# Optimization experiments

Measured on AMD Instinct MI355X. Metric: run time of the kernel, lower is better.

Reference implementation:

```python
import jax, jax.numpy as jnp
import numpy as np

VOCAB = 32000; D_MODEL = 768; N_LAYERS = 4
D_STATE = 16; D_CONV = 4; EXPAND = 2
D_INNER = EXPAND * D_MODEL                 # 1536
DT_RANK = (D_MODEL + 15) // 16             # 48
BATCH = 2; SEQ = 1024


def setup_inputs():
    key = jax.random.key(0)
    ks = jax.random.split(key, 10)
    def nrm(k, shape, scale=0.02):
        return (jax.random.normal(k, shape) * scale).astype(jnp.float32)
    inp = {}
    inp['tokens'] = jax.random.randint(ks[0], (BATCH, SEQ), 0, VOCAB)
    inp['embedding'] = nrm(ks[1], (VOCAB, D_MODEL))
    inp['head_bias'] = jnp.zeros((VOCAB,), jnp.float32)
    inp['ln_g'] = jnp.ones((N_LAYERS, D_MODEL), jnp.float32)
    inp['ln_b'] = jnp.zeros((N_LAYERS, D_MODEL), jnp.float32)
    inp['W_in'] = nrm(ks[2], (N_LAYERS, 2 * D_INNER, D_MODEL))
    inp['conv_w'] = nrm(ks[3], (N_LAYERS, D_INNER, 1, D_CONV), 0.1)
    inp['conv_b'] = jnp.zeros((N_LAYERS, D_INNER), jnp.float32)
    inp['W_xproj'] = nrm(ks[4], (N_LAYERS, DT_RANK + 2 * D_STATE, D_INNER))
    inp['W_dt'] = nrm(ks[5], (N_LAYERS, D_INNER, DT_RANK), 0.1)
    inp['b_dt'] = nrm(ks[6], (N_LAYERS, D_INNER), 0.5)
    # S4D-real init: A_n = n for n in 1..d_state
    inp['A_log'] = jnp.broadcast_to(jnp.log(jnp.arange(1, D_STATE + 1, dtype=jnp.float32)), (N_LAYERS, D_INNER, D_STATE)).copy()
    inp['D_ssm'] = jnp.ones((N_LAYERS, D_INNER), jnp.float32)
    inp['W_out'] = nrm(ks[7], (N_LAYERS, D_MODEL, D_INNER))
    inp['norm_g'] = jnp.ones((D_MODEL,), jnp.float32)
    inp['norm_b'] = jnp.zeros((D_MODEL,), jnp.float32)
    return inp


def _ln(x, g, b):
    m = jnp.mean(x, axis=-1, keepdims=True)
    v = jnp.var(x, axis=-1, keepdims=True)
    return (x - m) * jax.lax.rsqrt(v + 1e-5) * g + b


def _mamba(x, W_in, conv_w, conv_b, W_xproj, W_dt, b_dt, A_log, D_ssm, W_out):
    # x: (S, B, D_MODEL)
    xz = jnp.einsum('sbd,ed->sbe', x, W_in)           # (S, B, 2*D_INNER)
    xc, z = jnp.split(xz, 2, axis=-1)
    # depthwise causal conv along sequence
    xt = jnp.transpose(xc, (1, 2, 0))                  # (B, C, S)
    xt = jax.lax.conv_general_dilated(xt, conv_w, (1,), [(D_CONV - 1, 0)],
                                      dimension_numbers=('NCH', 'OIH', 'NCH'),
                                      feature_group_count=D_INNER)
    xt = xt + conv_b[None, :, None]
    xc = jax.nn.silu(jnp.transpose(xt, (2, 0, 1)))     # (S, B, C)
    xdb = jnp.einsum('sbc,ec->sbe', xc, W_xproj)       # (S, B, DT_RANK+2N)
    dt_r = xdb[..., :DT_RANK]
    Bm = xdb[..., DT_RANK:DT_RANK + D_STATE]
    Cm = xdb[..., DT_RANK + D_STATE:]
    dt = jax.nn.softplus(jnp.einsum('sbr,cr->sbc', dt_r, W_dt) + b_dt)
    A = -jnp.exp(A_log)                                # (C, N)

    def step(h, t):
        dt_t, B_t, C_t, x_t = t                        # (B,C),(B,N),(B,N),(B,C)
        dA = jnp.exp(dt_t[..., None] * A)              # (B, C, N)
        h = h * dA + (dt_t * x_t)[..., None] * B_t[:, None, :]
        y = jnp.einsum('bcn,bn->bc', h, C_t)
        return h, y

    h0 = jnp.zeros((x.shape[1], D_INNER, D_STATE), x.dtype)
    _, ys = jax.lax.scan(step, h0, (dt, Bm, Cm, xc))   # ys: (S, B, C)
    y = (ys + D_ssm * xc) * jax.nn.silu(z)
    return jnp.einsum('sbc,dc->sbd', y, W_out)


def reference(tokens, embedding, head_bias, ln_g, ln_b, W_in, conv_w, conv_b, W_xproj, W_dt, b_dt, A_log, D_ssm, W_out, norm_g, norm_b):
    x = embedding[tokens.T]                            # (S, B, D)
    for i in range(N_LAYERS):
        x = x + _mamba(_ln(x, ln_g[i], ln_b[i]), W_in[i], conv_w[i], conv_b[i],
                       W_xproj[i], W_dt[i], b_dt[i], A_log[i], D_ssm[i], W_out[i])
    x = _ln(x, norm_g, norm_b)
    logits = jnp.einsum('sbd,vd->sbv', x, embedding) + head_bias  # tied head
    return jnp.transpose(logits, (1, 0, 2))            # (B, S, VOCAB)
```

## Files before the change

kernel.cpp:

```cpp
#include <hip/hip_runtime.h>
#include <hip/hip_bf16.h>
#include <cstdint>
#include <cstddef>

#define SEQ_LEN 1024
#define NBATCH  2
#define MROWS   2048
#define DMODEL  768
#define DINNER  1536
#define DTRANK  48
#define DSTATE  16
#define NLAYERS 4
#define NVOCAB  32000
#define XPROJ_N 80
#define NCHUNK  16
#define CHUNK   64
#define GROUPS  (NBATCH * DINNER)
#define SCANW   (GROUPS * DSTATE)

typedef __attribute__((ext_vector_type(4))) float f32x4;
typedef __attribute__((ext_vector_type(8))) short s16x8;
using bf16 = __hip_bfloat16;

__device__ __forceinline__ float b2f(bf16 v){ return __bfloat162float(v); }
__device__ __forceinline__ bf16  f2b(float v){ return __float2bfloat16(v); }
__device__ __forceinline__ short f2bs(float v){
  return (short)__builtin_bit_cast(unsigned short, __float2bfloat16(v));
}

__device__ __forceinline__ void glds16(const ushort* g, ushort* l) {
  __builtin_amdgcn_global_load_lds(
      (const __attribute__((address_space(1))) void*)g,
      (__attribute__((address_space(3))) void*)l,
      16, 0, 0);
}

__global__ __launch_bounds__(256) void k_cvt(const float* __restrict__ in,
    ushort* __restrict__ out, int n4) {
  int i = blockIdx.x * 256 + threadIdx.x;
  if (i >= n4) return;
  f32x4 v = *(const f32x4*)(in + (size_t)i * 4);
  ushort4 o;
  o.x = (ushort)f2bs(v[0]); o.y = (ushort)f2bs(v[1]);
  o.z = (ushort)f2bs(v[2]); o.w = (ushort)f2bs(v[3]);
  *(ushort4*)(out + (size_t)i * 4) = o;
}

__global__ __launch_bounds__(256) void k_zero(float* __restrict__ p, int n4) {
  int i = blockIdx.x * 256 + threadIdx.x;
  if (i >= n4) return;
  f32x4 z = {};
  *(f32x4*)(p + (size_t)i * 4) = z;
}

__global__ __launch_bounds__(256) void k_embed(const int* __restrict__ tok,
    const float* __restrict__ emb, float* __restrict__ x) {
  int id = blockIdx.x * 256 + threadIdx.x;
  int m = id / DMODEL, d = id - m * DMODEL;
  x[id] = emb[(size_t)tok[m] * DMODEL + d];
}

__global__ __launch_bounds__(256) void k_ln(const float* __restrict__ x,
    bf16* __restrict__ out, const float* __restrict__ g, const float* __restrict__ b) {
  int m = blockIdx.x;
  const float* row = x + (size_t)m * DMODEL;
  int t = threadIdx.x;
  float v0[3];
  float s = 0.f, s2 = 0.f;
#pragma unroll
  for (int j = 0; j < 3; j++) {
    float v = row[t + j * 256];
    v0[j] = v; s += v; s2 += v * v;
  }
#pragma unroll
  for (int o = 32; o >= 1; o >>= 1) { s += __shfl_xor(s, o); s2 += __shfl_xor(s2, o); }
  __shared__ float red[8];
  int wave = t >> 6;
  if ((t & 63) == 0) { red[wave] = s; red[4 + wave] = s2; }
  __syncthreads();
  s  = red[0] + red[1] + red[2] + red[3];
  s2 = red[4] + red[5] + red[6] + red[7];
  float mean = s * (1.f / DMODEL);
  float var  = s2 * (1.f / DMODEL) - mean * mean;
  float rstd = rsqrtf(var + 1e-5f);
#pragma unroll
  for (int j = 0; j < 3; j++) {
    int d = t + j * 256;
    float o = (v0[j] - mean) * rstd * g[d] + b[d];
    out[(size_t)m * DMODEL + d] = f2b(o);
  }
}

template<bool HAS_BIAS, bool ADD_TO_C, bool ATOMIC>
__global__ __launch_bounds__(256) void k_gemm128(
    const ushort* __restrict__ A, int lda,
    const ushort* __restrict__ B, int ldb,
    float* __restrict__ C, int ldc,
    const float* __restrict__ bias,
    int M, int N, int K)
{
  __shared__ ushort As[128 * 32];
  __shared__ ushort Bs[128 * 32];
  const int t = threadIdx.x;
  const int lane = t & 63;
  const int wave = t >> 6;
  const int tile_m = blockIdx.x * 128;
  const int tile_n = blockIdx.y * 128;
  const int kper = K / gridDim.z;
  const int kb = blockIdx.z * kper;
  const int ke = kb + kper;
  const int wr = (wave >> 1) * 64;
  const int wc = (wave & 1) * 64;

  f32x4 acc[4][4] = {};

  const int sr = wave * 32 + (lane >> 2);
  const int sc = (lane & 3) * 8;
  const ushort* gA0 = A + (size_t)(tile_m + sr) * lda + sc + kb;
  const ushort* gA1 = gA0 + (size_t)16 * lda;
  const ushort* gB0 = B + (size_t)(tile_n + sr) * ldb + sc + kb;
  const ushort* gB1 = gB0 + (size_t)16 * ldb;
  ushort* lA0 = As + wave * 1024;
  ushort* lA1 = As + wave * 1024 + 512;
  ushort* lB0 = Bs + wave * 1024;
  ushort* lB1 = Bs + wave * 1024 + 512;

  const int fr = lane & 15;
  const int kk = (lane >> 4) * 8;

  for (int k0 = kb; k0 < ke; k0 += 32) {
    glds16(gA0, lA0);
    glds16(gA1, lA1);
    glds16(gB0, lB0);
    glds16(gB1, lB1);
    gA0 += 32; gA1 += 32; gB0 += 32; gB1 += 32;
    __syncthreads();
    s16x8 a[4], b[4];
#pragma unroll
    for (int m = 0; m < 4; m++)
      a[m] = *(const s16x8*)&As[(wr + m * 16 + fr) * 32 + kk];
#pragma unroll
    for (int n = 0; n < 4; n++)
      b[n] = *(const s16x8*)&Bs[(wc + n * 16 + fr) * 32 + kk];
#pragma unroll
    for (int m = 0; m < 4; m++)
#pragma unroll
      for (int n = 0; n < 4; n++)
        acc[m][n] = __builtin_amdgcn_mfma_f32_16x16x32_bf16(a[m], b[n], acc[m][n], 0, 0, 0);
    __syncthreads();
  }

  const int rq = (lane >> 4) * 4;
#pragma unroll
  for (int m = 0; m < 4; m++)
#pragma unroll
    for (int n = 0; n < 4; n++) {
      int colg = tile_n + wc + n * 16 + fr;
      float bv = HAS_BIAS ? bias[colg] : 0.f;
#pragma unroll
      for (int r = 0; r < 4; r++) {
        int rowg = tile_m + wr + m * 16 + rq + r;
        size_t idx = (size_t)rowg * ldc + colg;
        float v = acc[m][n][r] + bv;
        if constexpr (ATOMIC) atomicAdd(&C[idx], v);
        else if constexpr (ADD_TO_C) C[idx] += v;
        else C[idx] = v;
      }
    }
}

template<int MODE>
__global__ __launch_bounds__(256) void k_gemm(
    const ushort* __restrict__ A, int lda,
    const ushort* __restrict__ W, int ldw,
    void* __restrict__ Cout, int ldc,
    int M, int N, int K,
    const float* __restrict__ bias,
    const float* __restrict__ xcp,
    float* __restrict__ dtxp)
{
  __shared__ ushort As[64][40];
  __shared__ ushort Ws[64][40];
  const int tile_m = blockIdx.x * 64;
  const int tile_n = blockIdx.y * 64;
  const int t = threadIdx.x;
  const int lane = t & 63;
  const int wave = t >> 6;
  const int wr = (wave >> 1) * 32;
  const int wc = (wave & 1) * 32;
  f32x4 acc[2][2] = {};

  const int kper = ((K + gridDim.z - 1) / gridDim.z + 31) & ~31;
  const int kb = blockIdx.z * kper;
  int ke = kb + kper; if (ke > K) ke = K;

  const int srow = t >> 2;
  const int scol = (t & 3) * 8;

  for (int k0 = kb; k0 < ke; k0 += 32) {
    {
      int gm = tile_m + srow, gk = k0 + scol;
      s16x8 v = {};
      if (gm < M) {
        if (gk + 8 <= K) v = *(const s16x8*)(A + (size_t)gm * lda + gk);
        else {
#pragma unroll
          for (int j = 0; j < 8; j++) if (gk + j < K) v[j] = (short)A[(size_t)gm * lda + gk + j];
        }
      }
      *(s16x8*)&As[srow][scol] = v;
    }
    {
      int gn = tile_n + srow, gk = k0 + scol;
      s16x8 v = {};
      if (gn < N) {
        if (gk + 8 <= K) v = *(const s16x8*)(W + (size_t)gn * ldw + gk);
        else {
#pragma unroll
          for (int j = 0; j < 8; j++) if (gk + j < K) v[j] = (short)W[(size_t)gn * ldw + gk + j];
        }
      }
      *(s16x8*)&Ws[srow][scol] = v;
    }
    __syncthreads();
    const int kk = (lane >> 4) * 8;
    const int fr = lane & 15;
    s16x8 a0 = *(const s16x8*)&As[wr + fr][kk];
    s16x8 a1 = *(const s16x8*)&As[wr + 16 + fr][kk];
    s16x8 b0 = *(const s16x8*)&Ws[wc + fr][kk];
    s16x8 b1 = *(const s16x8*)&Ws[wc + 16 + fr][kk];
    acc[0][0] = __builtin_amdgcn_mfma_f32_16x16x32_bf16(a0, b0, acc[0][0], 0, 0, 0);
    acc[0][1] = __builtin_amdgcn_mfma_f32_16x16x32_bf16(a0, b1, acc[0][1], 0, 0, 0);
    acc[1][0] = __builtin_amdgcn_mfma_f32_16x16x32_bf16(a1, b0, acc[1][0], 0, 0, 0);
    acc[1][1] = __builtin_amdgcn_mfma_f32_16x16x32_bf16(a1, b1, acc[1][1], 0, 0, 0);
    __syncthreads();
  }

  const int fr = lane & 15;
  const int rq = (lane >> 4) * 4;
#pragma unroll
  for (int i = 0; i < 2; i++)
#pragma unroll
    for (int j = 0; j < 2; j++) {
      int colg = tile_n + wc + j * 16 + fr;
#pragma unroll
      for (int r = 0; r < 4; r++) {
        int rowg = tile_m + wr + i * 16 + rq + r;
        if (rowg < M && colg < N) {
          float v = acc[i][j][r];
          size_t idx = (size_t)rowg * ldc + colg;
          if constexpr (MODE == 0) {
            ((bf16*)Cout)[idx] = f2b(v);
          } else if constexpr (MODE == 2) {
            v += bias[colg];
            float sp = (v > 20.f) ? v : log1pf(__expf(v));
            ((float*)Cout)[idx] = sp;
            dtxp[idx] = sp * xcp[idx];
          } else {
            atomicAdd((float*)Cout + idx, v);
          }
        }
      }
    }
}

__global__ __launch_bounds__(256) void k_conv(const float* __restrict__ xz,
    const float* __restrict__ w, const float* __restrict__ cb,
    float* __restrict__ xc, bf16* __restrict__ xcb) {
  int id = blockIdx.x * 256 + threadIdx.x;
  int m = id / DINNER, c = id - m * DINNER;
  int s = m & (SEQ_LEN - 1);
  float acc = cb[c];
#pragma unroll
  for (int k = 0; k < 4; k++) {
    int sp = s - 3 + k;
    if (sp >= 0) acc += w[c * 4 + k] * xz[(size_t)(m - 3 + k) * (2 * DINNER) + c];
  }
  float sil = acc / (1.f + __expf(-acc));
  xc[id] = sil;
  xcb[id] = f2b(sil);
}

__global__ __launch_bounds__(256) void k_scan1(const float* __restrict__ dt,
    const float* __restrict__ dtx, const bf16* __restrict__ xdb,
    const float* __restrict__ A_log, float* __restrict__ aprod,
    float* __restrict__ hend) {
  int gid = blockIdx.x * 256 + threadIdx.x;
  int n  = gid & 15;
  int t2 = gid >> 4;
  int j  = t2 / GROUPS;
  int cb = t2 - j * GROUPS;
  int c  = cb % DINNER;
  int b  = cb / DINNER;
  float Acn = -__expf(A_log[c * DSTATE + n]);
  float h = 0.f, ap = 1.f;
  int mbase = b * SEQ_LEN + j * CHUNK;
#pragma unroll 4
  for (int s = 0; s < CHUNK; s++) {
    int m = mbase + s;
    float dtv = dt[(size_t)m * DINNER + c];
    float dxv = dtx[(size_t)m * DINNER + c];
    float Bv  = b2f(xdb[(size_t)m * XPROJ_N + DTRANK + n]);
    float dA  = __expf(dtv * Acn);
    h = h * dA + dxv * Bv;
    ap *= dA;
  }
  aprod[gid] = ap;
  hend[gid]  = h;
}

__global__ __launch_bounds__(256) void k_scan2(const float* __restrict__ aprod,
    const float* __restrict__ hend, float* __restrict__ hin) {
  int idx = blockIdx.x * 256 + threadIdx.x;
  float h = 0.f;
#pragma unroll
  for (int j = 0; j < NCHUNK; j++) {
    hin[(size_t)j * SCANW + idx] = h;
    h = aprod[(size_t)j * SCANW + idx] * h + hend[(size_t)j * SCANW + idx];
  }
}

__global__ __launch_bounds__(256) void k_scan3(const float* __restrict__ dt,
    const float* __restrict__ dtx, const bf16* __restrict__ xdb,
    const float* __restrict__ A_log, const float* __restrict__ hin,
    float* __restrict__ y) {
  int gid = blockIdx.x * 256 + threadIdx.x;
  int n  = gid & 15;
  int t2 = gid >> 4;
  int j  = t2 / GROUPS;
  int cb = t2 - j * GROUPS;
  int c  = cb % DINNER;
  int b  = cb / DINNER;
  float Acn = -__expf(A_log[c * DSTATE + n]);
  float h = hin[gid];
  int mbase = b * SEQ_LEN + j * CHUNK;
#pragma unroll 2
  for (int s = 0; s < CHUNK; s++) {
    int m = mbase + s;
    float dtv = dt[(size_t)m * DINNER + c];
    float dxv = dtx[(size_t)m * DINNER + c];
    float Bv  = b2f(xdb[(size_t)m * XPROJ_N + DTRANK + n]);
    float Cv  = b2f(xdb[(size_t)m * XPROJ_N + DTRANK + DSTATE + n]);
    float dA  = __expf(dtv * Acn);
    h = h * dA + dxv * Bv;
    float p = h * Cv;
    p += __shfl_xor(p, 8);
    p += __shfl_xor(p, 4);
    p += __shfl_xor(p, 2);
    p += __shfl_xor(p, 1);
    if (n == 0) y[(size_t)m * DINNER + c] = p;
  }
}

__global__ __launch_bounds__(256) void k_ycomb(const float* __restrict__ y,
    const float* __restrict__ xc, const float* __restrict__ xz,
    const float* __restrict__ D_ssm, bf16* __restrict__ ybf) {
  int id = blockIdx.x * 256 + threadIdx.x;
  int m = id / DINNER, c = id - m * DINNER;
  float z = xz[(size_t)m * (2 * DINNER) + DINNER + c];
  float sil = z / (1.f + __expf(-z));
  float v = (y[id] + D_ssm[c] * xc[id]) * sil;
  ybf[id] = f2b(v);
}

extern "C" void kernel_launch(void* const* d_in, const int* in_sizes, int n_in,
                              void* d_out, int out_size, void* d_ws, size_t ws_size,
                              hipStream_t stream) {
  const int*   tokens    = (const int*)  d_in[0];
  const float* embedding = (const float*)d_in[1];
  const float* head_bias = (const float*)d_in[2];
  const float* ln_g      = (const float*)d_in[3];
  const float* ln_b      = (const float*)d_in[4];
  const float* W_in      = (const float*)d_in[5];
  const float* conv_w    = (const float*)d_in[6];
  const float* conv_b    = (const float*)d_in[7];
  const float* W_xproj   = (const float*)d_in[8];
  const float* W_dt      = (const float*)d_in[9];
  const float* b_dt      = (const float*)d_in[10];
  const float* A_log     = (const float*)d_in[11];
  const float* D_ssm     = (const float*)d_in[12];
  const float* W_out     = (const float*)d_in[13];
  const float* norm_g    = (const float*)d_in[14];
  const float* norm_b    = (const float*)d_in[15];
  float* out = (float*)d_out;

  char* ws = (char*)d_ws;
  size_t off = 0;
  auto alloc = [&](size_t bytes) -> char* {
    char* p = ws + off;
    off = (off + bytes + 255) & ~(size_t)255;
    return p;
  };
  float*  x     = (float*) alloc((size_t)MROWS * DMODEL * 4);
  bf16*   xln   = (bf16*)  alloc((size_t)MROWS * DMODEL * 2);
  float*  xz    = (float*) alloc((size_t)MROWS * 2 * DINNER * 4);
  float*  xc    = (float*) alloc((size_t)MROWS * DINNER * 4);
  bf16*   xcb   = (bf16*)  alloc((size_t)MROWS * DINNER * 2);
  bf16*   xdb   = (bf16*)  alloc((size_t)MROWS * XPROJ_N * 2);
  float*  xdbf  = (float*) alloc((size_t)MROWS * XPROJ_N * 4);
  float*  dtf   = (float*) alloc((size_t)MROWS * DINNER * 4);
  float*  dtx   = (float*) alloc((size_t)MROWS * DINNER * 4);
  float*  yraw  = (float*) alloc((size_t)MROWS * DINNER * 4);
  bf16*   ybf   = (bf16*)  alloc((size_t)MROWS * DINNER * 2);
  float*  aprod = (float*) alloc((size_t)SCANW * NCHUNK * 4);
  float*  hend  = (float*) alloc((size_t)SCANW * NCHUNK * 4);
  float*  hin   = (float*) alloc((size_t)SCANW * NCHUNK * 4);
  ushort* ebf   = (ushort*)alloc((size_t)NVOCAB * DMODEL * 2);
  ushort* winb  = (ushort*)alloc((size_t)NLAYERS * 2 * DINNER * DMODEL * 2);
  ushort* wxpb  = (ushort*)alloc((size_t)NLAYERS * XPROJ_N * DINNER * 2);
  ushort* wdtb  = (ushort*)alloc((size_t)NLAYERS * DINNER * DTRANK * 2);
  ushort* woutb = (ushort*)alloc((size_t)NLAYERS * DMODEL * DINNER * 2);
  (void)ws_size; (void)in_sizes; (void)n_in; (void)out_size;

  auto cvt = [&](const float* src, ushort* dst, size_t n) {
    int n4 = (int)(n / 4);
    k_cvt<<<(n4 + 255) / 256, 256, 0, stream>>>(src, dst, n4);
  };
  cvt(embedding, ebf,   (size_t)NVOCAB * DMODEL);
  cvt(W_in,      winb,  (size_t)NLAYERS * 2 * DINNER * DMODEL);
  cvt(W_xproj,   wxpb,  (size_t)NLAYERS * XPROJ_N * DINNER);
  cvt(W_dt,      wdtb,  (size_t)NLAYERS * DINNER * DTRANK);
  cvt(W_out,     woutb, (size_t)NLAYERS * DMODEL * DINNER);

  k_embed<<<MROWS * DMODEL / 256, 256, 0, stream>>>(tokens, embedding, x);

  const int XDBN4 = MROWS * XPROJ_N / 4;

  for (int L = 0; L < NLAYERS; L++) {
    k_ln<<<MROWS, 256, 0, stream>>>(x, xln, ln_g + L * DMODEL, ln_b + L * DMODEL);

    k_gemm128<false, false, false><<<dim3(MROWS / 128, (2 * DINNER) / 128), 256, 0, stream>>>(
        (const ushort*)xln, DMODEL,
        winb + (size_t)L * 2 * DINNER * DMODEL, DMODEL,
        xz, 2 * DINNER, nullptr, MROWS, 2 * DINNER, DMODEL);

    k_conv<<<MROWS * DINNER / 256, 256, 0, stream>>>(
        xz, conv_w + (size_t)L * DINNER * 4, conv_b + (size_t)L * DINNER, xc, xcb);

    k_zero<<<(XDBN4 + 255) / 256, 256, 0, stream>>>(xdbf, XDBN4);
    k_gemm<3><<<dim3(MROWS / 64, 2, 8), 256, 0, stream>>>(
        (const ushort*)xcb, DINNER,
        wxpb + (size_t)L * XPROJ_N * DINNER, DINNER,
        (void*)xdbf, XPROJ_N, MROWS, XPROJ_N, DINNER,
        nullptr, nullptr, nullptr);
    k_cvt<<<(XDBN4 + 255) / 256, 256, 0, stream>>>(xdbf, (ushort*)xdb, XDBN4);

    k_gemm<2><<<dim3(MROWS / 64, DINNER / 64), 256, 0, stream>>>(
        (const ushort*)xdb, XPROJ_N,
        wdtb + (size_t)L * DINNER * DTRANK, DTRANK,
        (void*)dtf, DINNER, MROWS, DINNER, DTRANK,
        b_dt + (size_t)L * DINNER, xc, dtx);

    const float* Al = A_log + (size_t)L * DINNER * DSTATE;
    k_scan1<<<SCANW * NCHUNK / 256, 256, 0, stream>>>(dtf, dtx, xdb, Al, aprod, hend);
    k_scan2<<<SCANW / 256, 256, 0, stream>>>(aprod, hend, hin);
    k_scan3<<<SCANW * NCHUNK / 256, 256, 0, stream>>>(dtf, dtx, xdb, Al, hin, yraw);

    k_ycomb<<<MROWS * DINNER / 256, 256, 0, stream>>>(
        yraw, xc, xz, D_ssm + (size_t)L * DINNER, ybf);

    k_gemm128<false, true, true><<<dim3(MROWS / 128, DMODEL / 128, 4), 256, 0, stream>>>(
        (const ushort*)ybf, DINNER,
        woutb + (size_t)L * DMODEL * DINNER, DINNER,
        x, DMODEL, nullptr, MROWS, DMODEL, DINNER);
  }

  k_ln<<<MROWS, 256, 0, stream>>>(x, xln, norm_g, norm_b);

  k_gemm128<true, false, false><<<dim3(MROWS / 128, NVOCAB / 128), 256, 0, stream>>>(
      (const ushort*)xln, DMODEL,
      ebf, DMODEL,
      out, NVOCAB, head_bias, MROWS, NVOCAB, DMODEL);
}
```

Measured before the change: 1.050 ms.

## Double-buffer gemm128 LDS loads and replace x_proj atomics with split-K reduction

The 128x128 GEMM now keeps two LDS buffers and issues the global-to-LDS loads for the next K slice before computing the current one. It waits on vmcnt and uses raw s_barrier so load latency overlaps MFMA work, at the cost of doubled LDS use and possibly lower occupancy. Separately, the x_proj split-K GEMM writes per-split partial results to a scratch buffer instead of doing atomicAdd. A new kernel sums the partials and converts to bf16, which removes the zero-fill kernel and atomic contention in exchange for extra scratch memory traffic.

```diff
diff --git a/kernel.cpp b/kernel.cpp
--- a/kernel.cpp
+++ b/kernel.cpp
@@ -17,6 +17,7 @@
 #define CHUNK   64
 #define GROUPS  (NBATCH * DINNER)
 #define SCANW   (GROUPS * DSTATE)
+#define XSPLIT  8
 
 typedef __attribute__((ext_vector_type(4))) float f32x4;
 typedef __attribute__((ext_vector_type(8))) short s16x8;
@@ -46,11 +47,20 @@
   *(ushort4*)(out + (size_t)i * 4) = o;
 }
 
-__global__ __launch_bounds__(256) void k_zero(float* __restrict__ p, int n4) {
+__global__ __launch_bounds__(256) void k_xsum(const float* __restrict__ p,
+    ushort* __restrict__ out, int n4) {
   int i = blockIdx.x * 256 + threadIdx.x;
   if (i >= n4) return;
-  f32x4 z = {};
-  *(f32x4*)(p + (size_t)i * 4) = z;
+  f32x4 s = {};
+#pragma unroll
+  for (int z = 0; z < XSPLIT; z++) {
+    f32x4 v = *(const f32x4*)(p + (size_t)z * (MROWS * XPROJ_N) + (size_t)i * 4);
+    s[0] += v[0]; s[1] += v[1]; s[2] += v[2]; s[3] += v[3];
+  }
+  ushort4 o;
+  o.x = (ushort)f2bs(s[0]); o.y = (ushort)f2bs(s[1]);
+  o.z = (ushort)f2bs(s[2]); o.w = (ushort)f2bs(s[3]);
+  *(ushort4*)(out + (size_t)i * 4) = o;
 }
 
 __global__ __launch_bounds__(256) void k_embed(const int* __restrict__ tok,
@@ -99,8 +109,8 @@
     const float* __restrict__ bias,
     int M, int N, int K)
 {
-  __shared__ ushort As[128 * 32];
-  __shared__ ushort Bs[128 * 32];
+  __shared__ ushort As[2][128 * 32];
+  __shared__ ushort Bs[2][128 * 32];
   const int t = threadIdx.x;
   const int lane = t & 63;
   const int wave = t >> 6;
@@ -120,34 +130,45 @@
   const ushort* gA1 = gA0 + (size_t)16 * lda;
   const ushort* gB0 = B + (size_t)(tile_n + sr) * ldb + sc + kb;
   const ushort* gB1 = gB0 + (size_t)16 * ldb;
-  ushort* lA0 = As + wave * 1024;
-  ushort* lA1 = As + wave * 1024 + 512;
-  ushort* lB0 = Bs + wave * 1024;
-  ushort* lB1 = Bs + wave * 1024 + 512;
 
   const int fr = lane & 15;
   const int kk = (lane >> 4) * 8;
 
+  auto stage = [&](int bb) {
+    glds16(gA0, &As[bb][wave * 1024]);
+    glds16(gA1, &As[bb][wave * 1024 + 512]);
+    glds16(gB0, &Bs[bb][wave * 1024]);
+    glds16(gB1, &Bs[bb][wave * 1024 + 512]);
+    gA0 += 32; gA1 += 32; gB0 += 32; gB1 += 32;
+  };
+
+  stage(0);
+  int cur = 0;
+
   for (int k0 = kb; k0 < ke; k0 += 32) {
-    glds16(gA0, lA0);
-    glds16(gA1, lA1);
-    glds16(gB0, lB0);
-    glds16(gB1, lB1);
-    gA0 += 32; gA1 += 32; gB0 += 32; gB1 += 32;
-    __syncthreads();
+    if (k0 + 32 < ke) {
+      stage(cur ^ 1);
+      asm volatile("s_waitcnt vmcnt(4)" ::: "memory");
+    } else {
+      asm volatile("s_waitcnt vmcnt(0)" ::: "memory");
+    }
+    __builtin_amdgcn_s_barrier();
+
     s16x8 a[4], b[4];
 #pragma unroll
     for (int m = 0; m < 4; m++)
-      a[m] = *(const s16x8*)&As[(wr + m * 16 + fr) * 32 + kk];
+      a[m] = *(const s16x8*)&As[cur][(wr + m * 16 + fr) * 32 + kk];
 #pragma unroll
     for (int n = 0; n < 4; n++)
-      b[n] = *(const s16x8*)&Bs[(wc + n * 16 + fr) * 32 + kk];
+      b[n] = *(const s16x8*)&Bs[cur][(wc + n * 16 + fr) * 32 + kk];
 #pragma unroll
     for (int m = 0; m < 4; m++)
 #pragma unroll
       for (int n = 0; n < 4; n++)
         acc[m][n] = __builtin_amdgcn_mfma_f32_16x16x32_bf16(a[m], b[n], acc[m][n], 0, 0, 0);
-    __syncthreads();
+
+    __builtin_amdgcn_s_barrier();
+    cur ^= 1;
   }
 
   const int rq = (lane >> 4) * 4;
@@ -257,7 +278,7 @@
             ((float*)Cout)[idx] = sp;
             dtxp[idx] = sp * xcp[idx];
           } else {
-            atomicAdd((float*)Cout + idx, v);
+            ((float*)Cout)[(size_t)blockIdx.z * (MROWS * XPROJ_N) + idx] = v;
           }
         }
       }
@@ -397,7 +418,7 @@
   float*  xc    = (float*) alloc((size_t)MROWS * DINNER * 4);
   bf16*   xcb   = (bf16*)  alloc((size_t)MROWS * DINNER * 2);
   bf16*   xdb   = (bf16*)  alloc((size_t)MROWS * XPROJ_N * 2);
-  float*  xdbf  = (float*) alloc((size_t)MROWS * XPROJ_N * 4);
+  float*  xdbp  = (float*) alloc((size_t)XSPLIT * MROWS * XPROJ_N * 4);
   float*  dtf   = (float*) alloc((size_t)MROWS * DINNER * 4);
   float*  dtx   = (float*) alloc((size_t)MROWS * DINNER * 4);
   float*  yraw  = (float*) alloc((size_t)MROWS * DINNER * 4);
@@ -437,13 +458,12 @@
     k_conv<<<MROWS * DINNER / 256, 256, 0, stream>>>(
         xz, conv_w + (size_t)L * DINNER * 4, conv_b + (size_t)L * DINNER, xc, xcb);
 
-    k_zero<<<(XDBN4 + 255) / 256, 256, 0, stream>>>(xdbf, XDBN4);
-    k_gemm<3><<<dim3(MROWS / 64, 2, 8), 256, 0, stream>>>(
+    k_gemm<3><<<dim3(MROWS / 64, 2, XSPLIT), 256, 0, stream>>>(
         (const ushort*)xcb, DINNER,
         wxpb + (size_t)L * XPROJ_N * DINNER, DINNER,
-        (void*)xdbf, XPROJ_N, MROWS, XPROJ_N, DINNER,
+        (void*)xdbp, XPROJ_N, MROWS, XPROJ_N, DINNER,
         nullptr, nullptr, nullptr);
-    k_cvt<<<(XDBN4 + 255) / 256, 256, 0, stream>>>(xdbf, (ushort*)xdb, XDBN4);
+    k_xsum<<<(XDBN4 + 255) / 256, 256, 0, stream>>>(xdbp, (ushort*)xdb, XDBN4);
 
     k_gemm<2><<<dim3(MROWS / 64, DINNER / 64), 256, 0, stream>>>(
         (const ushort*)xdb, XPROJ_N,
```

Measured after the change: 1.014 ms. 1.04x faster.
